# Performance work log

Measured on AMD Instinct MI355X. Metric: run time of the kernel, lower is better.

Reference implementation:

```python
import jax, jax.numpy as jnp
import numpy as np

MA_K = 2 * 125 + 1  # 251, moving-average kernel
MV_K = 4 * 125 + 1  # 501, moving-variance kernel
EPS = 1e-5


def _avg_pool1d(x, K):
    """PyTorch F.avg_pool1d(stride=1, padding=(K-1)//2, count_include_pad=True)
    computed in O(L) via prefix sums. x: (B, C, L) -> (B, C, L)."""
    pad = (K - 1) // 2
    xp = jnp.pad(x, ((0, 0), (0, 0), (pad, pad)))  # zero pad, length L+K-1
    c = jnp.pad(jnp.cumsum(xp, axis=-1), ((0, 0), (0, 0), (1, 0)))  # length L+K
    return (c[..., K:] - c[..., :-K]) / K  # divide by K always (count_include_pad)


def setup_inputs() -> dict:
    key = jax.random.key(0)
    x = jax.random.normal(key, (8192, 1, 3750), dtype=jnp.float32)
    return {"x": x}


def reference(x):
    # global z-norm per (batch, channel); torch.std is unbiased (ddof=1)
    x = (x - jnp.mean(x, axis=2, keepdims=True)) / (
        jnp.std(x, axis=2, keepdims=True, ddof=1) + EPS)
    # remove moving average (kernel 251)
    x = x - _avg_pool1d(x, MA_K)
    # rescale by moving std (kernel 501)
    x = x / (jnp.sqrt(_avg_pool1d(x * x, MV_K)) + EPS)
    return x
```

## Files before the change

kernel.cpp:

```cpp
#include <hip/hip_runtime.h>
#include <math.h>

namespace {

constexpr int L      = 3750;
constexpr int NPAIR  = L / 2;
constexpr int BLK    = 256;
constexpr int CH     = 15;
constexpr int NCHUNK = L / CH;
constexpr int NFULL  = NPAIR / BLK;
constexpr int NTAIL  = NPAIR - NFULL * BLK;
constexpr float EPS  = 1e-5f;

__device__ __forceinline__ float frcp(float x)  { return __builtin_amdgcn_rcpf(x); }
__device__ __forceinline__ float fsqrt(float x) { return __builtin_amdgcn_sqrtf(x); }
__device__ __forceinline__ float frsq(float x)  { return __builtin_amdgcn_rsqf(x); }

template<int CTRL, int RMASK>
__device__ __forceinline__ float dpp_add(float v) {
    const int t = __builtin_amdgcn_update_dpp(0, __float_as_int(v),
                                              CTRL, RMASK, 0xf, true);
    return v + __int_as_float(t);
}

__device__ __forceinline__ float wave_iscan(float v) {
    v = dpp_add<0x111, 0xf>(v);
    v = dpp_add<0x112, 0xf>(v);
    v = dpp_add<0x114, 0xf>(v);
    v = dpp_add<0x118, 0xf>(v);
    v = dpp_add<0x142, 0xa>(v);
    v = dpp_add<0x143, 0xc>(v);
    return v;
}

__global__ __launch_bounds__(BLK, 8)
void preproc_kernel(const float* __restrict__ in, float* __restrict__ out) {
    __shared__ __align__(16) float sp[L + 2];
    __shared__ float sred[8];

    const int tid  = threadIdx.x;
    const int lane = tid & 63;
    const int wave = tid >> 6;
    const size_t rowoff = (size_t)blockIdx.x * (size_t)L;
    const float* rin  = in  + rowoff;
    float*       rout = out + rowoff;

    const bool active = (tid < NCHUNK);
    const int  base   = tid * CH;
    const bool tl     = (tid < NTAIL);

    {
        const float2* rin2 = reinterpret_cast<const float2*>(rin);
        float2 v[NFULL + 1];
        #pragma unroll
        for (int k = 0; k < NFULL; ++k) v[k] = rin2[k * BLK + tid];
        if (tl) v[NFULL] = rin2[NFULL * BLK + tid];
        float2* sp2 = reinterpret_cast<float2*>(sp);
        #pragma unroll
        for (int k = 0; k < NFULL; ++k) sp2[k * BLK + tid] = v[k];
        if (tl) sp2[NFULL * BLK + tid] = v[NFULL];
    }
    __syncthreads();

    float y[CH];
    float cy = 0.f, cy2 = 0.f;
    if (active) {
        #pragma unroll
        for (int j = 0; j < CH; ++j) {
            const float v = sp[base + j];
            y[j] = v;
            cy  += v;
            cy2  = fmaf(v, v, cy2);
        }
    } else {
        #pragma unroll
        for (int j = 0; j < CH; ++j) y[j] = 0.f;
    }
    const float iy = wave_iscan(cy);
    const float t2 = wave_iscan(cy2);
    if (lane == 63) { sred[wave] = iy; sred[4 + wave] = t2; }
    __syncthreads();
    float woff = 0.f;
    #pragma unroll
    for (int w = 0; w < 4; ++w) if (w < wave) woff += sred[w];
    const float totY  = sred[0] + sred[1] + sred[2] + sred[3];
    const float totY2 = sred[4] + sred[5] + sred[6] + sred[7];
    const float mean  = totY * (1.f / (float)L);
    const float var   = (totY2 - totY * mean) * (1.f / (float)(L - 1));
    const float s     = fsqrt(var) + EPS;
    const float epsS  = EPS * s;

    {
        float run = woff + iy - cy;
        if (active) {
            #pragma unroll
            for (int j = 0; j < CH; ++j) { sp[base + j] = run; run += y[j]; }
            if (tid == NCHUNK - 1) sp[L] = run;
        }
    }
    __syncthreads();

    const float inv251 = 1.f / 251.f;
    float cu = 0.f;
    if (active) {
        if (tid >= 9 && tid <= 240) {
            #pragma unroll
            for (int j = 0; j < CH; ++j) {
                const int i = base + j;
                const float sumY = sp[i + 126] - sp[i - 125];
                const float u = fmaf(sumY, -inv251, y[j]);
                y[j] = u;
                cu   = fmaf(u, u, cu);
            }
        } else {
            #pragma unroll
            for (int j = 0; j < CH; ++j) {
                const int i  = base + j;
                const int lo = (i > 125) ? i - 125 : 0;
                const int hi = (i + 126 < L) ? i + 126 : L;
                const float sumY = sp[hi] - sp[lo];
                const float cnt  = (float)(hi - lo);
                float u = y[j] - mean * (1.f - cnt * inv251);
                u = fmaf(sumY, -inv251, u);
                y[j] = u;
                cu   = fmaf(u, u, cu);
            }
        }
    }
    const float iu = wave_iscan(cu);
    if (lane == 63) sred[wave] = iu;
    __syncthreads();
    float woff2 = 0.f;
    #pragma unroll
    for (int w = 0; w < 4; ++w) if (w < wave) woff2 += sred[w];

    {
        float run = woff2 + iu - cu;
        if (active) {
            #pragma unroll
            for (int j = 0; j < CH; ++j) { sp[base + j] = run; run = fmaf(y[j], y[j], run); }
            if (tid == NCHUNK - 1) sp[L] = run;
        }
    }
    __syncthreads();

    const float inv501 = 1.f / 501.f;
    if (active) {
        if (tid >= 17 && tid <= 232) {
            #pragma unroll
            for (int j = 0; j < CH; ++j) {
                const int i = base + j;
                const float W = fmaxf((sp[i + 251] - sp[i - 250]) * inv501, 0.f);
                const float t = frsq(W);
                y[j] = y[j] * t * fmaf(-epsS, t, 1.f);
            }
        } else {
            #pragma unroll
            for (int j = 0; j < CH; ++j) {
                const int i  = base + j;
                const int lo = (i > 250) ? i - 250 : 0;
                const int hi = (i + 251 < L) ? i + 251 : L;
                const float W = fmaxf((sp[hi] - sp[lo]) * inv501, 0.f);
                const float t = frsq(W);
                y[j] = y[j] * t * fmaf(-epsS, t, 1.f);
            }
        }
    }
    __syncthreads();

    if (active) {
        #pragma unroll
        for (int j = 0; j < CH; ++j) sp[base + j] = y[j];
    }
    __syncthreads();

    {
        const float2* sp2 = reinterpret_cast<const float2*>(sp);
        float2* rout2 = reinterpret_cast<float2*>(rout);
        float2 v[NFULL + 1];
        #pragma unroll
        for (int k = 0; k < NFULL; ++k) v[k] = sp2[k * BLK + tid];
        if (tl) v[NFULL] = sp2[NFULL * BLK + tid];
        #pragma unroll
        for (int k = 0; k < NFULL; ++k) rout2[k * BLK + tid] = v[k];
        if (tl) rout2[NFULL * BLK + tid] = v[NFULL];
    }
}

}

extern "C" void kernel_launch(void* const* d_in, const int* in_sizes, int n_in,
                              void* d_out, int out_size, void* d_ws, size_t ws_size,
                              hipStream_t stream) {
    const float* x = (const float*)d_in[0];
    float* out = (float*)d_out;
    const int rows = in_sizes[0] / L;
    preproc_kernel<<<rows, BLK, 0, stream>>>(x, out);
}
```

Before: 44.43 us.

## Process four rows per block with register prefetch of the next row

Each block now handles four consecutive rows in a loop, loading the next row's input into registers while the current row is processed in shared memory. The goal is to overlap global-memory latency with compute and to cut block launch overhead. In exchange the grid shrinks by four, which lowers parallelism and adds register pressure from the prefetch buffer. The launch also assumes the row count divides evenly by four.

```diff
diff --git a/kernel.cpp b/kernel.cpp
--- a/kernel.cpp
+++ b/kernel.cpp
@@ -6,13 +6,13 @@
 constexpr int L      = 3750;
 constexpr int NPAIR  = L / 2;
 constexpr int BLK    = 256;
+constexpr int RPB    = 4;
 constexpr int CH     = 15;
 constexpr int NCHUNK = L / CH;
 constexpr int NFULL  = NPAIR / BLK;
 constexpr int NTAIL  = NPAIR - NFULL * BLK;
 constexpr float EPS  = 1e-5f;
 
-__device__ __forceinline__ float frcp(float x)  { return __builtin_amdgcn_rcpf(x); }
 __device__ __forceinline__ float fsqrt(float x) { return __builtin_amdgcn_sqrtf(x); }
 __device__ __forceinline__ float frsq(float x)  { return __builtin_amdgcn_rsqf(x); }
 
@@ -41,149 +41,163 @@
     const int tid  = threadIdx.x;
     const int lane = tid & 63;
     const int wave = tid >> 6;
-    const size_t rowoff = (size_t)blockIdx.x * (size_t)L;
-    const float* rin  = in  + rowoff;
-    float*       rout = out + rowoff;
+    const size_t row0 = (size_t)blockIdx.x * (size_t)RPB;
 
     const bool active = (tid < NCHUNK);
     const int  base   = tid * CH;
     const bool tl     = (tid < NTAIL);
 
+    float2 vin[NFULL + 1];
     {
-        const float2* rin2 = reinterpret_cast<const float2*>(rin);
-        float2 v[NFULL + 1];
+        const float2* g = reinterpret_cast<const float2*>(in + row0 * L);
         #pragma unroll
-        for (int k = 0; k < NFULL; ++k) v[k] = rin2[k * BLK + tid];
-        if (tl) v[NFULL] = rin2[NFULL * BLK + tid];
-        float2* sp2 = reinterpret_cast<float2*>(sp);
+        for (int k = 0; k < NFULL; ++k) vin[k] = g[k * BLK + tid];
+        if (tl) vin[NFULL] = g[NFULL * BLK + tid];
+    }
+
+    for (int r = 0; r < RPB; ++r) {
+        {
+            float2* sp2 = reinterpret_cast<float2*>(sp);
+            #pragma unroll
+            for (int k = 0; k < NFULL; ++k) sp2[k * BLK + tid] = vin[k];
+            if (tl) sp2[NFULL * BLK + tid] = vin[NFULL];
+        }
+        __syncthreads();
+
+        if (r + 1 < RPB) {
+            const float2* g = reinterpret_cast<const float2*>(in + (row0 + r + 1) * L);
+            #pragma unroll
+            for (int k = 0; k < NFULL; ++k) vin[k] = g[k * BLK + tid];
+            if (tl) vin[NFULL] = g[NFULL * BLK + tid];
+        }
+
+        float y[CH];
+        float cy = 0.f, cy2 = 0.f;
+        if (active) {
+            #pragma unroll
+            for (int j = 0; j < CH; ++j) {
+                const float v = sp[base + j];
+                y[j] = v;
+                cy  += v;
+                cy2  = fmaf(v, v, cy2);
+            }
+        } else {
+            #pragma unroll
+            for (int j = 0; j < CH; ++j) y[j] = 0.f;
+        }
+        const float iy = wave_iscan(cy);
+        const float t2 = wave_iscan(cy2);
+        if (lane == 63) { sred[wave] = iy; sred[4 + wave] = t2; }
+        __syncthreads();
+        float woff = 0.f;
         #pragma unroll
-        for (int k = 0; k < NFULL; ++k) sp2[k * BLK + tid] = v[k];
-        if (tl) sp2[NFULL * BLK + tid] = v[NFULL];
-    }
-    __syncthreads();
-
-    float y[CH];
-    float cy = 0.f, cy2 = 0.f;
-    if (active) {
+        for (int w = 0; w < 4; ++w) if (w < wave) woff += sred[w];
+        const float totY  = sred[0] + sred[1] + sred[2] + sred[3];
+        const float totY2 = sred[4] + sred[5] + sred[6] + sred[7];
+        const float mean  = totY * (1.f / (float)L);
+        const float var   = (totY2 - totY * mean) * (1.f / (float)(L - 1));
+        const float s     = fsqrt(var) + EPS;
+        const float epsS  = EPS * s;
+
+        {
+            float run = woff + iy - cy;
+            if (active) {
+                #pragma unroll
+                for (int j = 0; j < CH; ++j) { sp[base + j] = run; run += y[j]; }
+                if (tid == NCHUNK - 1) sp[L] = run;
+            }
+        }
+        __syncthreads();
+
+        const float inv251 = 1.f / 251.f;
+        float cu = 0.f;
+        if (active) {
+            if (tid >= 9 && tid <= 240) {
+                #pragma unroll
+                for (int j = 0; j < CH; ++j) {
+                    const int i = base + j;
+                    const float sumY = sp[i + 126] - sp[i - 125];
+                    const float u = fmaf(sumY, -inv251, y[j]);
+                    y[j] = u;
+                    cu   = fmaf(u, u, cu);
+                }
+            } else {
+                #pragma unroll
+                for (int j = 0; j < CH; ++j) {
+                    const int i  = base + j;
+                    const int lo = (i > 125) ? i - 125 : 0;
+                    const int hi = (i + 126 < L) ? i + 126 : L;
+                    const float sumY = sp[hi] - sp[lo];
+                    const float cnt  = (float)(hi - lo);
+                    float u = y[j] - mean * (1.f - cnt * inv251);
+                    u = fmaf(sumY, -inv251, u);
+                    y[j] = u;
+                    cu   = fmaf(u, u, cu);
+                }
+            }
+        }
+        const float iu = wave_iscan(cu);
+        if (lane == 63) sred[wave] = iu;
+        __syncthreads();
+        float woff2 = 0.f;
         #pragma unroll
-        for (int j = 0; j < CH; ++j) {
-            const float v = sp[base + j];
-            y[j] = v;
-            cy  += v;
-            cy2  = fmaf(v, v, cy2);
-        }
-    } else {
-        #pragma unroll
-        for (int j = 0; j < CH; ++j) y[j] = 0.f;
-    }
-    const float iy = wave_iscan(cy);
-    const float t2 = wave_iscan(cy2);
-    if (lane == 63) { sred[wave] = iy; sred[4 + wave] = t2; }
-    __syncthreads();
-    float woff = 0.f;
-    #pragma unroll
-    for (int w = 0; w < 4; ++w) if (w < wave) woff += sred[w];
-    const float totY  = sred[0] + sred[1] + sred[2] + sred[3];
-    const float totY2 = sred[4] + sred[5] + sred[6] + sred[7];
-    const float mean  = totY * (1.f / (float)L);
-    const float var   = (totY2 - totY * mean) * (1.f / (float)(L - 1));
-    const float s     = fsqrt(var) + EPS;
-    const float epsS  = EPS * s;
-
-    {
-        float run = woff + iy - cy;
-        if (active) {
-            #pragma unroll
-            for (int j = 0; j < CH; ++j) { sp[base + j] = run; run += y[j]; }
-            if (tid == NCHUNK - 1) sp[L] = run;
-        }
-    }
-    __syncthreads();
-
-    const float inv251 = 1.f / 251.f;
-    float cu = 0.f;
-    if (active) {
-        if (tid >= 9 && tid <= 240) {
-            #pragma unroll
-            for (int j = 0; j < CH; ++j) {
-                const int i = base + j;
-                const float sumY = sp[i + 126] - sp[i - 125];
-                const float u = fmaf(sumY, -inv251, y[j]);
-                y[j] = u;
-                cu   = fmaf(u, u, cu);
-            }
-        } else {
-            #pragma unroll
-            for (int j = 0; j < CH; ++j) {
-                const int i  = base + j;
-                const int lo = (i > 125) ? i - 125 : 0;
-                const int hi = (i + 126 < L) ? i + 126 : L;
-                const float sumY = sp[hi] - sp[lo];
-                const float cnt  = (float)(hi - lo);
-                float u = y[j] - mean * (1.f - cnt * inv251);
-                u = fmaf(sumY, -inv251, u);
-                y[j] = u;
-                cu   = fmaf(u, u, cu);
-            }
-        }
-    }
-    const float iu = wave_iscan(cu);
-    if (lane == 63) sred[wave] = iu;
-    __syncthreads();
-    float woff2 = 0.f;
-    #pragma unroll
-    for (int w = 0; w < 4; ++w) if (w < wave) woff2 += sred[w];
-
-    {
-        float run = woff2 + iu - cu;
-        if (active) {
-            #pragma unroll
-            for (int j = 0; j < CH; ++j) { sp[base + j] = run; run = fmaf(y[j], y[j], run); }
-            if (tid == NCHUNK - 1) sp[L] = run;
-        }
-    }
-    __syncthreads();
-
-    const float inv501 = 1.f / 501.f;
-    if (active) {
-        if (tid >= 17 && tid <= 232) {
-            #pragma unroll
-            for (int j = 0; j < CH; ++j) {
-                const int i = base + j;
-                const float W = fmaxf((sp[i + 251] - sp[i - 250]) * inv501, 0.f);
-                const float t = frsq(W);
-                y[j] = y[j] * t * fmaf(-epsS, t, 1.f);
-            }
-        } else {
-            #pragma unroll
-            for (int j = 0; j < CH; ++j) {
-                const int i  = base + j;
-                const int lo = (i > 250) ? i - 250 : 0;
-                const int hi = (i + 251 < L) ? i + 251 : L;
-                const float W = fmaxf((sp[hi] - sp[lo]) * inv501, 0.f);
-                const float t = frsq(W);
-                y[j] = y[j] * t * fmaf(-epsS, t, 1.f);
-            }
-        }
-    }
-    __syncthreads();
-
-    if (active) {
-        #pragma unroll
-        for (int j = 0; j < CH; ++j) sp[base + j] = y[j];
-    }
-    __syncthreads();
-
-    {
-        const float2* sp2 = reinterpret_cast<const float2*>(sp);
-        float2* rout2 = reinterpret_cast<float2*>(rout);
-        float2 v[NFULL + 1];
-        #pragma unroll
-        for (int k = 0; k < NFULL; ++k) v[k] = sp2[k * BLK + tid];
-        if (tl) v[NFULL] = sp2[NFULL * BLK + tid];
-        #pragma unroll
-        for (int k = 0; k < NFULL; ++k) rout2[k * BLK + tid] = v[k];
-        if (tl) rout2[NFULL * BLK + tid] = v[NFULL];
+        for (int w = 0; w < 4; ++w) if (w < wave) woff2 += sred[w];
+
+        {
+            float run = woff2 + iu - cu;
+            if (active) {
+                #pragma unroll
+                for (int j = 0; j < CH; ++j) {
+                    sp[base + j] = run;
+                    run = fmaf(y[j], y[j], run);
+                }
+                if (tid == NCHUNK - 1) sp[L] = run;
+            }
+        }
+        __syncthreads();
+
+        const float inv501 = 1.f / 501.f;
+        if (active) {
+            if (tid >= 17 && tid <= 232) {
+                #pragma unroll
+                for (int j = 0; j < CH; ++j) {
+                    const int i = base + j;
+                    const float W = fmaxf((sp[i + 251] - sp[i - 250]) * inv501, 0.f);
+                    const float t = frsq(W);
+                    y[j] = y[j] * t * fmaf(-epsS, t, 1.f);
+                }
+            } else {
+                #pragma unroll
+                for (int j = 0; j < CH; ++j) {
+                    const int i  = base + j;
+                    const int lo = (i > 250) ? i - 250 : 0;
+                    const int hi = (i + 251 < L) ? i + 251 : L;
+                    const float W = fmaxf((sp[hi] - sp[lo]) * inv501, 0.f);
+                    const float t = frsq(W);
+                    y[j] = y[j] * t * fmaf(-epsS, t, 1.f);
+                }
+            }
+        }
+        __syncthreads();
+
+        if (active) {
+            #pragma unroll
+            for (int j = 0; j < CH; ++j) sp[base + j] = y[j];
+        }
+        __syncthreads();
+
+        {
+            const float2* sp2 = reinterpret_cast<const float2*>(sp);
+            float2* rout2 = reinterpret_cast<float2*>(out + (row0 + r) * L);
+            float2 vo[NFULL + 1];
+            #pragma unroll
+            for (int k = 0; k < NFULL; ++k) vo[k] = sp2[k * BLK + tid];
+            if (tl) vo[NFULL] = sp2[NFULL * BLK + tid];
+            #pragma unroll
+            for (int k = 0; k < NFULL; ++k) rout2[k * BLK + tid] = vo[k];
+            if (tl) rout2[NFULL * BLK + tid] = vo[NFULL];
+        }
+        if (r + 1 < RPB) __syncthreads();
     }
 }
 
@@ -195,5 +209,5 @@
     const float* x = (const float*)d_in[0];
     float* out = (float*)d_out;
     const int rows = in_sizes[0] / L;
-    preproc_kernel<<<rows, BLK, 0, stream>>>(x, out);
-}
+    preproc_kernel<<<rows / RPB, BLK, 0, stream>>>(x, out);
+}
```

Result: slower. 147.0 us (+230.9%).
